# Performance work log

Hardware: AMD Instinct MI355X
Metric: run time of the kernel (lower is better)

## Reference

```python
import jax, jax.numpy as jnp
import numpy as np


def setup_inputs() -> dict:
    key = jax.random.key(0)
    k1, k2, k3 = jax.random.split(key, 3)
    N, D, E = 4096, 1024, 8  # tokens, d_model, path_num (experts)
    x = jax.random.normal(k1, (N, D), dtype=jnp.float32)
    score = jax.random.uniform(k2, (N, E), dtype=jnp.float32)
    hot_mask = jax.random.randint(k3, (N, E), 0, 2).astype(jnp.int32)
    tag = jnp.arange(N, dtype=jnp.int32).reshape(N, 1)
    return {"x": x, "score": score, "hot_mask": hot_mask, "tag": tag}


def reference(x, score, hot_mask, tag):
    # Per-expert gather dispatch with score scaling (route_logic='1d', transform=True).
    # Torch version produces variable-length per-expert flows; here each expert's
    # output is packed into a fixed capacity of N slots (selected tokens first,
    # in original order, matching torch.nonzero ordering), zero-padded beyond count.
    N, D = x.shape
    E = hot_mask.shape[1]
    mask = hot_mask > 0  # [N, E] multi-hot routing mask
    pos = jnp.arange(N)

    def dispatch(mask_e, score_e):
        # stable partition: selected tokens get their index, others index+N
        order = jnp.argsort(jnp.where(mask_e, pos, pos + N))  # [N]
        count = mask_e.sum()
        valid = pos < count  # [N] first `count` slots hold real tokens
        data = x * score_e[:, None]  # transform: scale by routing score
        out_data = jnp.where(valid[:, None], data[order], 0.0)  # [N, D]
        out_tag = jnp.where(valid[:, None], tag[order], 0)      # [N, 1]
        return out_data, out_tag, count

    out_data, out_tags, counts = jax.vmap(dispatch, in_axes=(1, 1))(mask, score)
    # out_data: [E, N, D], out_tags: [E, N, 1], counts: [E]
    return out_data, out_tags, counts
```

## Files before the change

kernel.cpp:

```cpp
#include <hip/hip_runtime.h>

#define N_TOK 4096
#define DMODEL 1024
#define NEXP 8
#define BT 1024
#define TPB 4
#define PRPB 16

typedef float vfloat4 __attribute__((ext_vector_type(4)));

__global__ __launch_bounds__(BT) void build(
        const int* __restrict__ hot_mask,
        int* __restrict__ islot,
        int* __restrict__ cnt_i32,
        float* __restrict__ out_tags,
        float* __restrict__ out_cnts) {
    const int e = blockIdx.x;
    const int t = threadIdx.x;
    const int base = t * TPB;

    unsigned int bits = 0;
    int s = 0;
#pragma unroll
    for (int j = 0; j < TPB; ++j) {
        int m = (hot_mask[(size_t)(base + j) * NEXP + e] > 0) ? 1 : 0;
        bits |= (unsigned int)m << j;
        s += m;
    }

    __shared__ int sm[BT];
    sm[t] = s;
    __syncthreads();
    for (int off = 1; off < BT; off <<= 1) {
        int v = (t >= off) ? sm[t - off] : 0;
        __syncthreads();
        sm[t] += v;
        __syncthreads();
    }
    const int cnt = sm[BT - 1];
    int run = (t == 0) ? 0 : sm[t - 1];

#pragma unroll
    for (int j = 0; j < TPB; ++j) {
        const int tok = base + j;
        int sl = -1;
        if ((bits >> j) & 1u) {
            sl = run++;
            out_tags[e * N_TOK + sl] = (float)tok;
        }
        islot[tok * NEXP + e] = sl;
    }
    for (int slot = cnt + t; slot < N_TOK; slot += BT)
        out_tags[e * N_TOK + slot] = 0.0f;
    if (t == 0) {
        out_cnts[e] = (float)cnt;
        cnt_i32[e] = cnt;
    }
}

__global__ __launch_bounds__(256) void scatter_pad(
        const float* __restrict__ x,
        const float* __restrict__ score,
        const int* __restrict__ islot,
        const int* __restrict__ cnt_i32,
        float* __restrict__ out_data)
{
    const int b = blockIdx.x;
    const int t = threadIdx.x;
    const int n0 = 2 * b, n1 = 2 * b + 1;

    const vfloat4 v0 = reinterpret_cast<const vfloat4*>(x + (size_t)n0 * DMODEL)[t];
    const vfloat4 v1 = reinterpret_cast<const vfloat4*>(x + (size_t)n1 * DMODEL)[t];

#pragma unroll
    for (int e = 0; e < NEXP; ++e) {
        const int sl = islot[n0 * NEXP + e];
        if (sl >= 0) {
            vfloat4 w = v0 * score[n0 * NEXP + e];
            reinterpret_cast<vfloat4*>(
                out_data + ((size_t)e * N_TOK + sl) * DMODEL)[t] = w;
        }
    }
#pragma unroll
    for (int e = 0; e < NEXP; ++e) {
        const int sl = islot[n1 * NEXP + e];
        if (sl >= 0) {
            vfloat4 w = v1 * score[n1 * NEXP + e];
            reinterpret_cast<vfloat4*>(
                out_data + ((size_t)e * N_TOK + sl) * DMODEL)[t] = w;
        }
    }

    const int row0  = b * PRPB;
    const int e     = row0 >> 12;
    const int slot0 = row0 & (N_TOK - 1);
    const int cnt   = cnt_i32[e];
    if (slot0 + PRPB > cnt) {
        const vfloat4 z = (vfloat4)(0.f);
        for (int r = 0; r < PRPB; ++r) {
            if (slot0 + r < cnt) continue;
            reinterpret_cast<vfloat4*>(
                out_data + (size_t)(row0 + r) * DMODEL)[t] = z;
        }
    }
}

extern "C" void kernel_launch(void* const* d_in, const int* in_sizes, int n_in,
                              void* d_out, int out_size, void* d_ws, size_t ws_size,
                              hipStream_t stream) {
    const float* x        = (const float*)d_in[0];
    const float* score    = (const float*)d_in[1];
    const int*   hot_mask = (const int*)d_in[2];

    float* out      = (float*)d_out;
    float* out_data = out;
    float* out_tags = out + (size_t)NEXP * N_TOK * DMODEL;
    float* out_cnts = out_tags + (size_t)NEXP * N_TOK;

    int* islot   = (int*)d_ws;
    int* cnt_i32 = islot + N_TOK * NEXP;

    build<<<NEXP, BT, 0, stream>>>(hot_mask, islot, cnt_i32, out_tags, out_cnts);
    scatter_pad<<<N_TOK / 2, 256, 0, stream>>>(
        x, score, islot, cnt_i32, out_data);
}
```

Baseline: 34.36 us.

## Replace block-wide shared-memory scan with wave ballot/popcount prefix scan

The build kernel's Hillis-Steele scan over 1024 shared-memory entries needed about 20 block barriers. It is replaced by a per-wave ballot and popcount, followed by one 64-lane shuffle scan over the per-wave sums, which brings it down to two barriers. Tokens are now strided across threads, so each load instruction reads consecutive tokens, and slot ranks come from a popcount of the lower ballot bits. This should shorten the serial build kernel that runs before scatter_pad.

```diff
diff --git a/kernel.cpp b/kernel.cpp
--- a/kernel.cpp
+++ b/kernel.cpp
@@ -3,56 +3,60 @@
 #define N_TOK 4096
 #define DMODEL 1024
 #define NEXP 8
-#define BT 1024
-#define TPB 4
 #define PRPB 16
 
 typedef float vfloat4 __attribute__((ext_vector_type(4)));
 
-__global__ __launch_bounds__(BT) void build(
+__global__ __launch_bounds__(1024) void build(
         const int* __restrict__ hot_mask,
         int* __restrict__ islot,
         int* __restrict__ cnt_i32,
         float* __restrict__ out_tags,
         float* __restrict__ out_cnts) {
-    const int e = blockIdx.x;
-    const int t = threadIdx.x;
-    const int base = t * TPB;
+    const int e    = blockIdx.x;
+    const int tid  = threadIdx.x;
+    const int wave = tid >> 6;
+    const int lane = tid & 63;
 
-    unsigned int bits = 0;
-    int s = 0;
+    __shared__ int wsum[64];
+
+    unsigned long long bal[4];
 #pragma unroll
-    for (int j = 0; j < TPB; ++j) {
-        int m = (hot_mask[(size_t)(base + j) * NEXP + e] > 0) ? 1 : 0;
-        bits |= (unsigned int)m << j;
-        s += m;
+    for (int j = 0; j < 4; ++j) {
+        const int tok = j * 1024 + tid;
+        const int m = (hot_mask[(size_t)tok * NEXP + e] > 0) ? 1 : 0;
+        bal[j] = __ballot(m);
+        if (lane == 0) wsum[j * 16 + wave] = (int)__popcll(bal[j]);
     }
+    __syncthreads();
 
-    __shared__ int sm[BT];
-    sm[t] = s;
+    if (wave == 0) {
+        int v = wsum[lane];
+#pragma unroll
+        for (int off = 1; off < 64; off <<= 1) {
+            int u = __shfl_up(v, off);
+            if (lane >= off) v += u;
+        }
+        wsum[lane] = v;
+    }
     __syncthreads();
-    for (int off = 1; off < BT; off <<= 1) {
-        int v = (t >= off) ? sm[t - off] : 0;
-        __syncthreads();
-        sm[t] += v;
-        __syncthreads();
-    }
-    const int cnt = sm[BT - 1];
-    int run = (t == 0) ? 0 : sm[t - 1];
+    const int cnt = wsum[63];
 
 #pragma unroll
-    for (int j = 0; j < TPB; ++j) {
-        const int tok = base + j;
+    for (int j = 0; j < 4; ++j) {
+        const int tok = j * 1024 + tid;
+        const int idx = j * 16 + wave;
         int sl = -1;
-        if ((bits >> j) & 1u) {
-            sl = run++;
+        if ((bal[j] >> lane) & 1ull) {
+            sl = (idx ? wsum[idx - 1] : 0)
+               + (int)__popcll(bal[j] & ((1ull << lane) - 1ull));
             out_tags[e * N_TOK + sl] = (float)tok;
         }
         islot[tok * NEXP + e] = sl;
     }
-    for (int slot = cnt + t; slot < N_TOK; slot += BT)
+    for (int slot = cnt + tid; slot < N_TOK; slot += 1024)
         out_tags[e * N_TOK + slot] = 0.0f;
-    if (t == 0) {
+    if (tid == 0) {
         out_cnts[e] = (float)cnt;
         cnt_i32[e] = cnt;
     }
@@ -120,7 +124,7 @@
     int* islot   = (int*)d_ws;
     int* cnt_i32 = islot + N_TOK * NEXP;
 
-    build<<<NEXP, BT, 0, stream>>>(hot_mask, islot, cnt_i32, out_tags, out_cnts);
+    build<<<NEXP, 1024, 0, stream>>>(hot_mask, islot, cnt_i32, out_tags, out_cnts);
     scatter_pad<<<N_TOK / 2, 256, 0, stream>>>(
         x, score, islot, cnt_i32, out_data);
 }
```

Result: faster. 32.84 us (-4.4%).
